# Performance work log

Hardware: AMD Instinct MI355X
Metric: run time of the kernel (lower is better)

## Reference

```python
import jax, jax.numpy as jnp
import numpy as np

DIM = 1024
NUM_HEADS = 16
HEAD_DIM = DIM // NUM_HEADS
SCALE = HEAD_DIM ** -0.5


def setup_inputs() -> dict:
    key = jax.random.key(0)
    k1, k2, k3, k4, k5, k6 = jax.random.split(key, 6)
    B, S, L = 4, 8192, 512
    x = jax.random.normal(k1, (B, S, DIM), dtype=jnp.float32)
    latents = jax.random.normal(k2, (B, L, DIM), dtype=jnp.float32)
    # Linear weights stored torch-style as (out_features, in_features)
    w_q = jax.random.normal(k3, (DIM, DIM), dtype=jnp.float32) * (DIM ** -0.5)
    w_kv = jax.random.normal(k4, (2 * DIM, DIM), dtype=jnp.float32) * (DIM ** -0.5)
    w_out = jax.random.normal(k5, (DIM, DIM), dtype=jnp.float32) * (DIM ** -0.5)
    b_out = jax.random.normal(k6, (DIM,), dtype=jnp.float32) * 0.01
    return {"x": x, "latents": latents, "w_q": w_q, "w_kv": w_kv,
            "w_out": w_out, "b_out": b_out}


def reference(x, latents, w_q, w_kv, w_out, b_out):
    B, L, _ = latents.shape
    S = x.shape[1]
    q = latents @ w_q.T                      # (B, L, dim)
    kv = x @ w_kv.T                          # (B, S, 2*dim)
    k, v = jnp.split(kv, 2, axis=-1)         # each (B, S, dim)
    q = q.reshape(B, L, NUM_HEADS, HEAD_DIM)
    k = k.reshape(B, S, NUM_HEADS, HEAD_DIM)
    v = v.reshape(B, S, NUM_HEADS, HEAD_DIM)
    # attention scores: (B, H, L, S)
    attn = jnp.einsum('blhd,bshd->bhls', q, k) * SCALE
    attn = jax.nn.softmax(attn, axis=-1)
    out = jnp.einsum('bhls,bshd->blhd', attn, v)  # (B, L, H, D)
    out = out.reshape(B, L, DIM)
    return out @ w_out.T + b_out
```

## Files before the change

kernel.cpp:

```cpp
#include <hip/hip_runtime.h>
#include <hip/hip_bf16.h>
#include <cstdint>
#include <cstddef>

#define B_ 4
#define S_ 8192
#define L_ 512
#define DIM 1024
#define NUM_HEADS 16
#define HEAD_DIM 64
#define SCHUNK 4096
#define NSEG 2
#define SEGKEYS (SCHUNK / NSEG)
#define SCALE 0.125f
#define L2E 1.44269504088896f
#define F_SC (SCALE * L2E)

typedef __bf16 bf16;
typedef __bf16 bf16x8 __attribute__((ext_vector_type(8)));
typedef float f32x4 __attribute__((ext_vector_type(4)));

#define AS1 __attribute__((address_space(1)))
#define AS3 __attribute__((address_space(3)))
#define GLDS(g, l) __builtin_amdgcn_global_load_lds((const AS1 void*)(g), (AS3 void*)(l), 16, 0, 0)
#define LGKM_FENCE() asm volatile("s_waitcnt lgkmcnt(0)" ::: "memory")
#define VMCNT4() asm volatile("s_waitcnt vmcnt(4)" ::: "memory")
#define VMCNT0() asm volatile("s_waitcnt vmcnt(0)" ::: "memory")
#define MFMA16(a, b, c) __builtin_amdgcn_mfma_f32_16x16x32_bf16((a), (b), (c), 0, 0, 0)

__global__ void detect_dtype(const unsigned int* __restrict__ x, int* __restrict__ flag) {
  int lane = threadIdx.x;
  int cnt = 0;
  for (int i = 0; i < 4; ++i) {
    unsigned int w = x[lane * 4 + i];
    unsigned int e = (w >> 7) & 0xFFu;
    cnt += (e >= 117u && e <= 129u) ? 1 : 0;
  }
  cnt += __shfl_xor(cnt, 1);
  cnt += __shfl_xor(cnt, 2);
  cnt += __shfl_xor(cnt, 4);
  cnt += __shfl_xor(cnt, 8);
  cnt += __shfl_xor(cnt, 16);
  cnt += __shfl_xor(cnt, 32);
  if (lane == 0) *flag = (cnt < 128) ? 1 : 0;
}

template<int REMAP>
__global__ __launch_bounds__(256) void conv_bf16(
    const void* __restrict__ in, bf16* __restrict__ out, int nchunk, int srow0,
    const int* __restrict__ flagp)
{
  const bool f32in = (*flagp != 0);
  for (int c = blockIdx.x * 256 + threadIdx.x; c < nchunk; c += gridDim.x * 256) {
    size_t gc;
    if (REMAP) {
      int r = c >> 7, cc = c & 127;
      gc = ((size_t)((r >> 12) * 8192 + srow0 + (r & 4095)) << 7) + cc;
    } else {
      gc = (size_t)c;
    }
    if (f32in) {
      const f32x4* g = (const f32x4*)in + gc * 2;
      f32x4 lo = g[0], hi = g[1];
      bf16x8 w;
      w[0] = (bf16)lo[0]; w[1] = (bf16)lo[1]; w[2] = (bf16)lo[2]; w[3] = (bf16)lo[3];
      w[4] = (bf16)hi[0]; w[5] = (bf16)hi[1]; w[6] = (bf16)hi[2]; w[7] = (bf16)hi[3];
      *(bf16x8*)(out + (size_t)c * 8) = w;
    } else {
      *(bf16x8*)(out + (size_t)c * 8) = ((const bf16x8*)in)[gc];
    }
  }
}

template<int HAS_BIAS, int DUAL_OUT, int NBN>
__global__ __launch_bounds__(256) void gemm_nt(
    const bf16* __restrict__ Ap, const bf16* __restrict__ Bwp,
    void* __restrict__ Cp, const void* __restrict__ biasp,
    int M, int N, int K, const int* __restrict__ flagp)
{
  __shared__ __align__(16) bf16 lA[128 * 64];
  __shared__ __align__(16) bf16 lB[128 * 64];
  const int tid = threadIdx.x;
  const int lane = tid & 63, quad = lane >> 4, l16 = lane & 15, wave = tid >> 6;
  const int wm = wave >> 1, wn = wave & 1;
  const int f = blockIdx.x;
  const int xcd = f & 7, sidx = f >> 3;
  const int bn = sidx % NBN;
  const int bm = xcd * (M >> 10) + sidx / NBN;
  const bool f32in = (HAS_BIAS || DUAL_OUT) ? (*flagp != 0) : false;

  f32x4 acc[4][4] = {};
  const int nK = K >> 6;
  for (int kb = 0; kb < nK; ++kb) {
    __syncthreads();
#pragma unroll
    for (int i = 0; i < 4; ++i) {
      int e = i * 256 + tid;
      int row = e >> 3, cp = e & 7, gcp = cp ^ (row & 7);
      const bf16* ga = Ap + (size_t)(bm * 128 + row) * K + kb * 64 + gcp * 8;
      GLDS(ga, lA + e * 8);
      const bf16* gb = Bwp + (size_t)(bn * 128 + row) * K + kb * 64 + gcp * 8;
      GLDS(gb, lB + e * 8);
    }
    __syncthreads();

#pragma unroll
    for (int ks = 0; ks < 2; ++ks) {
      bf16x8 af[4], bfr[4];
#pragma unroll
      for (int t = 0; t < 4; ++t) {
        int rowA = wm * 64 + t * 16 + l16;
        int ca = (ks * 4 + quad) ^ (rowA & 7);
        af[t] = *(const bf16x8*)(lA + rowA * 64 + ca * 8);
        int rowB = wn * 64 + t * 16 + l16;
        int cb = (ks * 4 + quad) ^ (rowB & 7);
        bfr[t] = *(const bf16x8*)(lB + rowB * 64 + cb * 8);
      }
#pragma unroll
      for (int tm = 0; tm < 4; ++tm)
#pragma unroll
        for (int tn = 0; tn < 4; ++tn)
          acc[tm][tn] = MFMA16(af[tm], bfr[tn], acc[tm][tn]);
    }
  }

#pragma unroll
  for (int tn = 0; tn < 4; ++tn) {
    int col = bn * 128 + wn * 64 + tn * 16 + l16;
    float bv = 0.0f;
    if (HAS_BIAS)
      bv = f32in ? ((const float*)biasp)[col] : (float)((const bf16*)biasp)[col];
#pragma unroll
    for (int tm = 0; tm < 4; ++tm) {
#pragma unroll
      for (int r = 0; r < 4; ++r) {
        int rowc = bm * 128 + wm * 64 + tm * 16 + quad * 4 + r;
        float v = acc[tm][tn][r] + bv;
        if (DUAL_OUT && f32in) {
          ((float*)Cp)[(size_t)rowc * N + col] = v;
        } else {
          ((bf16*)Cp)[(size_t)rowc * N + col] = (bf16)v;
        }
      }
    }
  }
}

__global__ __launch_bounds__(512) void gemm_kv_256(
    const bf16* __restrict__ Ap, const bf16* __restrict__ Bwp,
    bf16* __restrict__ Cp, bf16* __restrict__ C2p, int M, int K)
{
  __shared__ __align__(16) bf16 lA[2][256 * 64];
  __shared__ __align__(16) bf16 lB[2][256 * 64];
  const int tid = threadIdx.x;
  const int lane = tid & 63, quad = lane >> 4, l16 = lane & 15, wave = tid >> 6;
  const int wm = wave >> 2, wn = wave & 3;
  const int f = blockIdx.x;
  const int xcd = f & 7, sidx = f >> 3;
  const int bn = sidx & 7;
  const int bm = xcd * ((M >> 8) >> 3) + (sidx >> 3);
  const int nK = K >> 6;

#define STAGE_A(buf, half, kb) do {                                          \
  _Pragma("unroll")                                                          \
  for (int j = 0; j < 2; ++j) {                                              \
    int e = j * 512 + tid;                                                   \
    int row = e >> 3, cp = e & 7, gcp = cp ^ (row & 7);                      \
    const bf16* g = Ap + (size_t)(bm * 256 + (half) * 128 + row) * K         \
                       + (kb) * 64 + gcp * 8;                                \
    GLDS(g, &lA[buf][((half) * 128 + row) * 64 + cp * 8]);                   \
  } } while (0)
#define STAGE_B(buf, half, kb) do {                                          \
  _Pragma("unroll")                                                          \
  for (int j = 0; j < 2; ++j) {                                              \
    int e = j * 512 + tid;                                                   \
    int row = e >> 3, cp = e & 7, gcp = cp ^ (row & 7);                      \
    const bf16* g = Bwp + (size_t)(bn * 256 + (half) * 128 + row) * K        \
                        + (kb) * 64 + gcp * 8;                               \
    GLDS(g, &lB[buf][((half) * 128 + row) * 64 + cp * 8]);                   \
  } } while (0)

  f32x4 acc[8][4] = {};

  STAGE_A(0, 0, 0); STAGE_A(0, 1, 0); STAGE_B(0, 0, 0); STAGE_B(0, 1, 0);
  if (nK > 1) { STAGE_B(1, 0, 1); STAGE_B(1, 1, 1); VMCNT4(); }
  else VMCNT0();
  __builtin_amdgcn_s_barrier();

  for (int t = 0; t < nK; ++t) {
    const int cur = t & 1;
    bf16x8 breg[4][2];
#pragma unroll
    for (int p = 0; p < 4; ++p) {
      bf16x8 af[2][2];
      if (p == 0) {
#pragma unroll
        for (int nf = 0; nf < 4; ++nf)
#pragma unroll
          for (int ks = 0; ks < 2; ++ks) {
            int rowB = wn * 64 + nf * 16 + l16;
            int cb = (ks * 4 + quad) ^ (rowB & 7);
            breg[nf][ks] = *(const bf16x8*)&lB[cur][rowB * 64 + cb * 8];
          }
      }
#pragma unroll
      for (int mf2 = 0; mf2 < 2; ++mf2)
#pragma unroll
        for (int ks = 0; ks < 2; ++ks) {
          int rowA = wm * 128 + (p * 2 + mf2) * 16 + l16;
          int ca = (ks * 4 + quad) ^ (rowA & 7);
          af[mf2][ks] = *(const bf16x8*)&lA[cur][rowA * 64 + ca * 8];
        }
      LGKM_FENCE();

      if (p == 0) { if (t + 1 < nK) STAGE_A(cur ^ 1, 0, t + 1); }
      else if (p == 1) { if (t + 1 < nK) STAGE_A(cur ^ 1, 1, t + 1); }
      else if (p == 2) { if (t + 2 < nK) STAGE_B(cur, 0, t + 2); }
      else             { if (t + 2 < nK) STAGE_B(cur, 1, t + 2); }

      __builtin_amdgcn_s_barrier();

      __builtin_amdgcn_s_setprio(1);
#pragma unroll
      for (int mf2 = 0; mf2 < 2; ++mf2)
#pragma unroll
        for (int nf = 0; nf < 4; ++nf)
#pragma unroll
          for (int ks = 0; ks < 2; ++ks)
            acc[p * 2 + mf2][nf] = MFMA16(af[mf2][ks], breg[nf][ks], acc[p * 2 + mf2][nf]);
      __builtin_amdgcn_s_setprio(0);
    }
    if (t + 1 < nK) {
      if (t + 2 < nK) VMCNT4(); else VMCNT0();
      __builtin_amdgcn_s_barrier();
    }
  }

#pragma unroll
  for (int tn = 0; tn < 4; ++tn) {
    int col = bn * 256 + wn * 64 + tn * 16 + l16;
    bf16* outp = (col < 1024) ? Cp : C2p;
    int ocol = col & 1023;
#pragma unroll
    for (int tm = 0; tm < 8; ++tm)
#pragma unroll
      for (int r = 0; r < 4; ++r) {
        int rowc = bm * 256 + wm * 128 + tm * 16 + quad * 4 + r;
        outp[(size_t)rowc * 1024 + ocol] = (bf16)acc[tm][tn][r];
      }
  }
#undef STAGE_A
#undef STAGE_B
}

template<int FIRST>
__global__ __launch_bounds__(256) void attn_pass(
    const bf16* __restrict__ qb, const bf16* __restrict__ kc, const bf16* __restrict__ vc,
    float* __restrict__ Ost, float* __restrict__ lst)
{
  __shared__ __align__(16) bf16 lK[64 * 64];
  __shared__ __align__(16) bf16 lV[64][72];
  __shared__ __align__(16) bf16 pbuf[4][16][72];
  const int tid = threadIdx.x;
  const int lane = tid & 63, quad = lane >> 4, l16 = lane & 15, wave = tid >> 6;
  const int f = blockIdx.x;
  const int xcd = f & 7, sidx = f >> 3;
  const int lt = sidx & 7, ghi = sidx >> 3;
  const int g = ghi * 8 + xcd;
  const int h = g & 15, bs = g >> 4;
  const int b = bs >> 1, seg = bs & 1;
  const int l0 = lt * 64 + wave * 16;

  const bf16* qbase = qb + (size_t)(b * L_ + l0 + l16) * DIM + h * HEAD_DIM + quad * 8;
  bf16x8 qf0 = *(const bf16x8*)qbase;
  bf16x8 qf1 = *(const bf16x8*)(qbase + 32);

  f32x4 acc[4] = {};
  float lsum[4] = {0.0f, 0.0f, 0.0f, 0.0f};

  const int sbeg = seg * SEGKEYS;
  for (int s0 = sbeg; s0 < sbeg + SEGKEYS; s0 += 64) {
    __syncthreads();
    for (int i = 0; i < 2; ++i) {
      int e = i * 256 + tid;
      int row = e >> 3, cp = e & 7, gcp = cp ^ (row & 7);
      const bf16* gk = kc + (size_t)(b * SCHUNK + s0 + row) * DIM + h * HEAD_DIM + gcp * 8;
      GLDS(gk, lK + e * 8);
    }
    for (int i = 0; i < 2; ++i) {
      int e = i * 256 + tid;
      int row = e >> 3, cc = e & 7;
      bf16x8 vv = *(const bf16x8*)(vc + (size_t)(b * SCHUNK + s0 + row) * DIM + h * HEAD_DIM + cc * 8);
      int pg = (row >> 3) ^ cc;
#pragma unroll
      for (int j = 0; j < 8; ++j)
        lV[cc * 8 + j][pg * 8 + (row & 7)] = vv[j];
    }
    __syncthreads();

    f32x4 sc[4];
#pragma unroll
    for (int kt = 0; kt < 4; ++kt) {
      int rk = kt * 16 + l16;
      int p0c = quad ^ (rk & 7);
      int p1c = (4 + quad) ^ (rk & 7);
      bf16x8 kf0 = *(const bf16x8*)(lK + rk * 64 + p0c * 8);
      bf16x8 kf1 = *(const bf16x8*)(lK + rk * 64 + p1c * 8);
      f32x4 s4 = {};
      s4 = MFMA16(qf0, kf0, s4);
      s4 = MFMA16(qf1, kf1, s4);
      sc[kt] = s4;
    }

#pragma unroll
    for (int r = 0; r < 4; ++r) {
      float a0 = exp2f(fminf(sc[0][r] * F_SC, 40.0f));
      float a1 = exp2f(fminf(sc[1][r] * F_SC, 40.0f));
      float a2 = exp2f(fminf(sc[2][r] * F_SC, 40.0f));
      float a3 = exp2f(fminf(sc[3][r] * F_SC, 40.0f));
      lsum[r] += a0 + a1 + a2 + a3;
      pbuf[wave][quad * 4 + r][l16]      = (bf16)a0;
      pbuf[wave][quad * 4 + r][16 + l16] = (bf16)a1;
      pbuf[wave][quad * 4 + r][32 + l16] = (bf16)a2;
      pbuf[wave][quad * 4 + r][48 + l16] = (bf16)a3;
    }
    LGKM_FENCE();
#pragma unroll
    for (int half = 0; half < 2; ++half) {
      bf16x8 pf = *(const bf16x8*)&pbuf[wave][l16][half * 32 + quad * 8];
#pragma unroll
      for (int t4 = 0; t4 < 4; ++t4) {
        int c = t4 * 16 + l16;
        int pg = (half * 4 + quad) ^ (c >> 3);
        bf16x8 vf = *(const bf16x8*)&lV[c][pg * 8];
        acc[t4] = MFMA16(pf, vf, acc[t4]);
      }
    }
  }

#pragma unroll
  for (int r = 0; r < 4; ++r) {
    lsum[r] += __shfl_xor(lsum[r], 1, 16);
    lsum[r] += __shfl_xor(lsum[r], 2, 16);
    lsum[r] += __shfl_xor(lsum[r], 4, 16);
    lsum[r] += __shfl_xor(lsum[r], 8, 16);
  }

  float* Oseg = Ost + (size_t)seg * (B_ * L_ * DIM);
  float* lseg = lst + (size_t)seg * (B_ * NUM_HEADS * L_);
#pragma unroll
  for (int r = 0; r < 4; ++r) {
    int l = l0 + quad * 4 + r;
    if (l16 == 0) {
      int si = (b * NUM_HEADS + h) * L_ + l;
      if (FIRST) lseg[si] = lsum[r];
      else       lseg[si] += lsum[r];
    }
  }
#pragma unroll
  for (int t4 = 0; t4 < 4; ++t4)
#pragma unroll
    for (int r = 0; r < 4; ++r) {
      int l = l0 + quad * 4 + r;
      size_t oi = (size_t)(b * L_ + l) * DIM + h * HEAD_DIM + t4 * 16 + l16;
      if (FIRST) Oseg[oi] = acc[t4][r];
      else       Oseg[oi] += acc[t4][r];
    }
}

__global__ __launch_bounds__(256) void combine_kernel(
    const float* __restrict__ Ost, const float* __restrict__ lst, bf16* __restrict__ ao)
{
  int idx = (blockIdx.x * 256 + threadIdx.x) * 4;
  int d0 = idx & (DIM - 1);
  int row = idx >> 10;
  int b = row >> 9, l = row & (L_ - 1);
  int h = d0 >> 6;
  int si = (b * NUM_HEADS + h) * L_ + l;
  float lv = lst[si] + lst[B_ * NUM_HEADS * L_ + si];
  float linv = 1.0f / lv;
  f32x4 o0 = *(const f32x4*)(Ost + idx);
  f32x4 o1 = *(const f32x4*)(Ost + (size_t)(B_ * L_ * DIM) + idx);
#pragma unroll
  for (int j = 0; j < 4; ++j)
    ao[idx + j] = (bf16)((o0[j] + o1[j]) * linv);
}

extern "C" void kernel_launch(void* const* d_in, const int* in_sizes, int n_in,
                              void* d_out, int out_size, void* d_ws, size_t ws_size,
                              hipStream_t stream)
{
  (void)in_sizes; (void)n_in; (void)out_size; (void)ws_size;
  const void* x       = d_in[0];
  const void* latents = d_in[1];
  const void* w_q     = d_in[2];
  const void* w_kv    = d_in[3];
  const void* w_out   = d_in[4];
  const void* b_out   = d_in[5];

  char* ws = (char*)d_ws;
  int*   flag  = (int*)ws;
  bf16*  qb    = (bf16*)(ws + ((size_t)1   << 20));
  float* lst   = (float*)(ws + ((size_t)5  << 20));
  bf16*  ao    = (bf16*)(ws + ((size_t)6   << 20));
  float* Ost   = (float*)(ws + ((size_t)10 << 20));
  bf16*  kc    = (bf16*)(ws + ((size_t)26 << 20));
  bf16*  latb  = (bf16*)(ws + ((size_t)26 << 20));
  bf16*  wqb   = (bf16*)(ws + ((size_t)30 << 20));
  bf16*  vc    = (bf16*)(ws + ((size_t)58 << 20));
  bf16*  xcb   = (bf16*)(ws + ((size_t)90 << 20));
  bf16*  wkvb  = (bf16*)(ws + ((size_t)122 << 20));
  bf16*  woutb = (bf16*)(ws + ((size_t)122 << 20));

  detect_dtype<<<1, 64, 0, stream>>>((const unsigned int*)x, flag);

  const int Mx = B_ * SCHUNK;

  conv_bf16<0><<<1024, 256, 0, stream>>>(latents, latb, (B_ * L_ * DIM) / 8, 0, flag);
  conv_bf16<0><<<512,  256, 0, stream>>>(w_q, wqb, (DIM * DIM) / 8, 0, flag);
  conv_bf16<0><<<1024, 256, 0, stream>>>(w_kv, wkvb, (2 * DIM * DIM) / 8, 0, flag);

  gemm_nt<0, 0, 8><<<128, 256, 0, stream>>>(
      latb, wqb, qb, nullptr, B_ * L_, DIM, DIM, flag);

  conv_bf16<1><<<2048, 256, 0, stream>>>(x, xcb, (Mx * DIM) / 8, 0, flag);
  gemm_kv_256<<<512, 512, 0, stream>>>(xcb, wkvb, kc, vc, Mx, DIM);
  attn_pass<1><<<1024, 256, 0, stream>>>(qb, kc, vc, Ost, lst);

  conv_bf16<1><<<2048, 256, 0, stream>>>(x, xcb, (Mx * DIM) / 8, SCHUNK, flag);
  gemm_kv_256<<<512, 512, 0, stream>>>(xcb, wkvb, kc, vc, Mx, DIM);
  attn_pass<0><<<1024, 256, 0, stream>>>(qb, kc, vc, Ost, lst);

  conv_bf16<0><<<512, 256, 0, stream>>>(w_out, woutb, (DIM * DIM) / 8, 0, flag);
  combine_kernel<<<(B_ * L_ * DIM / 4) / 256, 256, 0, stream>>>(Ost, lst, ao);

  gemm_nt<1, 1, 8><<<128, 256, 0, stream>>>(
      ao, woutb, d_out, b_out, B_ * L_, DIM, DIM, flag);
}
```

Measured before the change: 567.9 us.

## Write V transposed from KV GEMM and double-buffer K/V loads in attention

The KV GEMM epilogue now writes V in a head-major transposed layout (b,h,d,s) with packed 4-element stores, so attention can load V tiles straight into LDS with async global-to-LDS loads instead of register loads followed by scattered transposing LDS writes. The attention loop double-buffers K and V tiles, prefetching the next tile while computing on the current one and using one barrier per iteration. This removes the per-element LDS transpose and overlaps global loads with MFMA work, at the cost of doubled LDS for K/V. The transposed V stores in the GEMM epilogue are strided across rows, which may make that store less coalesced.

```diff
diff --git a/kernel.cpp b/kernel.cpp
--- a/kernel.cpp
+++ b/kernel.cpp
@@ -18,6 +18,7 @@
 
 typedef __bf16 bf16;
 typedef __bf16 bf16x8 __attribute__((ext_vector_type(8)));
+typedef __bf16 bf16x4 __attribute__((ext_vector_type(4)));
 typedef float f32x4 __attribute__((ext_vector_type(4)));
 
 #define AS1 __attribute__((address_space(1)))
@@ -236,18 +237,33 @@
     }
   }
 
-#pragma unroll
-  for (int tn = 0; tn < 4; ++tn) {
-    int col = bn * 256 + wn * 64 + tn * 16 + l16;
-    bf16* outp = (col < 1024) ? Cp : C2p;
-    int ocol = col & 1023;
-#pragma unroll
-    for (int tm = 0; tm < 8; ++tm)
-#pragma unroll
-      for (int r = 0; r < 4; ++r) {
-        int rowc = bm * 256 + wm * 128 + tm * 16 + quad * 4 + r;
-        outp[(size_t)rowc * 1024 + ocol] = (bf16)acc[tm][tn][r];
+  if (bn < 4) {
+#pragma unroll
+    for (int tn = 0; tn < 4; ++tn) {
+      int col = bn * 256 + wn * 64 + tn * 16 + l16;
+#pragma unroll
+      for (int tm = 0; tm < 8; ++tm)
+#pragma unroll
+        for (int r = 0; r < 4; ++r) {
+          int rowc = bm * 256 + wm * 128 + tm * 16 + quad * 4 + r;
+          Cp[(size_t)rowc * 1024 + col] = (bf16)acc[tm][tn][r];
+        }
+    }
+  } else {
+#pragma unroll
+    for (int tn = 0; tn < 4; ++tn) {
+      int dv = bn * 256 + wn * 64 + tn * 16 + l16 - 1024;
+      int hh = dv >> 6, dd = dv & 63;
+#pragma unroll
+      for (int tm = 0; tm < 8; ++tm) {
+        int rowbase = bm * 256 + wm * 128 + tm * 16 + quad * 4;
+        int bb = rowbase >> 12, ss = rowbase & 4095;
+        bf16x4 pk;
+        pk[0] = (bf16)acc[tm][tn][0]; pk[1] = (bf16)acc[tm][tn][1];
+        pk[2] = (bf16)acc[tm][tn][2]; pk[3] = (bf16)acc[tm][tn][3];
+        *(bf16x4*)&C2p[(((size_t)((bb * 16 + hh) * 64 + dd)) << 12) + ss] = pk;
       }
+    }
   }
 #undef STAGE_A
 #undef STAGE_B
@@ -255,11 +271,11 @@
 
 template<int FIRST>
 __global__ __launch_bounds__(256) void attn_pass(
-    const bf16* __restrict__ qb, const bf16* __restrict__ kc, const bf16* __restrict__ vc,
+    const bf16* __restrict__ qb, const bf16* __restrict__ kc, const bf16* __restrict__ vt,
     float* __restrict__ Ost, float* __restrict__ lst)
 {
-  __shared__ __align__(16) bf16 lK[64 * 64];
-  __shared__ __align__(16) bf16 lV[64][72];
+  __shared__ __align__(16) bf16 lK[2][64 * 64];
+  __shared__ __align__(16) bf16 lV[2][64 * 64];
   __shared__ __align__(16) bf16 pbuf[4][16][72];
   const int tid = threadIdx.x;
   const int lane = tid & 63, quad = lane >> 4, l16 = lane & 15, wave = tid >> 6;
@@ -270,33 +286,37 @@
   const int h = g & 15, bs = g >> 4;
   const int b = bs >> 1, seg = bs & 1;
   const int l0 = lt * 64 + wave * 16;
+  const int sbeg = seg * SEGKEYS;
 
   const bf16* qbase = qb + (size_t)(b * L_ + l0 + l16) * DIM + h * HEAD_DIM + quad * 8;
   bf16x8 qf0 = *(const bf16x8*)qbase;
   bf16x8 qf1 = *(const bf16x8*)(qbase + 32);
 
+  const int r0 = tid >> 3, c0 = tid & 7, g0 = c0 ^ (r0 & 7);
+  const bf16* kg = kc + (((size_t)(b * SCHUNK + sbeg + r0)) << 10) + h * HEAD_DIM + g0 * 8;
+  const bf16* vg = vt + (((size_t)((b * 16 + h) * 64 + r0)) << 12) + sbeg + g0 * 8;
+
   f32x4 acc[4] = {};
   float lsum[4] = {0.0f, 0.0f, 0.0f, 0.0f};
 
-  const int sbeg = seg * SEGKEYS;
-  for (int s0 = sbeg; s0 < sbeg + SEGKEYS; s0 += 64) {
-    __syncthreads();
-    for (int i = 0; i < 2; ++i) {
-      int e = i * 256 + tid;
-      int row = e >> 3, cp = e & 7, gcp = cp ^ (row & 7);
-      const bf16* gk = kc + (size_t)(b * SCHUNK + s0 + row) * DIM + h * HEAD_DIM + gcp * 8;
-      GLDS(gk, lK + e * 8);
-    }
-    for (int i = 0; i < 2; ++i) {
-      int e = i * 256 + tid;
-      int row = e >> 3, cc = e & 7;
-      bf16x8 vv = *(const bf16x8*)(vc + (size_t)(b * SCHUNK + s0 + row) * DIM + h * HEAD_DIM + cc * 8);
-      int pg = (row >> 3) ^ cc;
-#pragma unroll
-      for (int j = 0; j < 8; ++j)
-        lV[cc * 8 + j][pg * 8 + (row & 7)] = vv[j];
-    }
-    __syncthreads();
+  {
+    bf16* lk = lK[0]; bf16* lv = lV[0];
+    GLDS(kg, lk + tid * 8); GLDS(kg + (32 << 10), lk + (256 + tid) * 8);
+    GLDS(vg, lv + tid * 8); GLDS(vg + (32 << 12), lv + (256 + tid) * 8);
+    kg += (64 << 10); vg += 64;
+  }
+  VMCNT0();
+  __syncthreads();
+
+  const int NT = SEGKEYS / 64;
+  for (int t = 0; t < NT; ++t) {
+    const int cur = t & 1;
+    if (t + 1 < NT) {
+      bf16* lk = lK[cur ^ 1]; bf16* lv = lV[cur ^ 1];
+      GLDS(kg, lk + tid * 8); GLDS(kg + (32 << 10), lk + (256 + tid) * 8);
+      GLDS(vg, lv + tid * 8); GLDS(vg + (32 << 12), lv + (256 + tid) * 8);
+      kg += (64 << 10); vg += 64;
+    }
 
     f32x4 sc[4];
 #pragma unroll
@@ -304,8 +324,8 @@
       int rk = kt * 16 + l16;
       int p0c = quad ^ (rk & 7);
       int p1c = (4 + quad) ^ (rk & 7);
-      bf16x8 kf0 = *(const bf16x8*)(lK + rk * 64 + p0c * 8);
-      bf16x8 kf1 = *(const bf16x8*)(lK + rk * 64 + p1c * 8);
+      bf16x8 kf0 = *(const bf16x8*)&lK[cur][rk * 64 + p0c * 8];
+      bf16x8 kf1 = *(const bf16x8*)&lK[cur][rk * 64 + p1c * 8];
       f32x4 s4 = {};
       s4 = MFMA16(qf0, kf0, s4);
       s4 = MFMA16(qf1, kf1, s4);
@@ -330,12 +350,15 @@
       bf16x8 pf = *(const bf16x8*)&pbuf[wave][l16][half * 32 + quad * 8];
 #pragma unroll
       for (int t4 = 0; t4 < 4; ++t4) {
-        int c = t4 * 16 + l16;
-        int pg = (half * 4 + quad) ^ (c >> 3);
-        bf16x8 vf = *(const bf16x8*)&lV[c][pg * 8];
+        int d = t4 * 16 + l16;
+        int cp = (half * 4 + quad) ^ (d & 7);
+        bf16x8 vf = *(const bf16x8*)&lV[cur][d * 64 + cp * 8];
         acc[t4] = MFMA16(pf, vf, acc[t4]);
       }
     }
+
+    VMCNT0();
+    __syncthreads();
   }
 
 #pragma unroll
@@ -407,7 +430,7 @@
   bf16*  kc    = (bf16*)(ws + ((size_t)26 << 20));
   bf16*  latb  = (bf16*)(ws + ((size_t)26 << 20));
   bf16*  wqb   = (bf16*)(ws + ((size_t)30 << 20));
-  bf16*  vc    = (bf16*)(ws + ((size_t)58 << 20));
+  bf16*  vt    = (bf16*)(ws + ((size_t)58 << 20));
   bf16*  xcb   = (bf16*)(ws + ((size_t)90 << 20));
   bf16*  wkvb  = (bf16*)(ws + ((size_t)122 << 20));
   bf16*  woutb = (bf16*)(ws + ((size_t)122 << 20));
@@ -424,12 +447,12 @@
       latb, wqb, qb, nullptr, B_ * L_, DIM, DIM, flag);
 
   conv_bf16<1><<<2048, 256, 0, stream>>>(x, xcb, (Mx * DIM) / 8, 0, flag);
-  gemm_kv_256<<<512, 512, 0, stream>>>(xcb, wkvb, kc, vc, Mx, DIM);
-  attn_pass<1><<<1024, 256, 0, stream>>>(qb, kc, vc, Ost, lst);
+  gemm_kv_256<<<512, 512, 0, stream>>>(xcb, wkvb, kc, vt, Mx, DIM);
+  attn_pass<1><<<1024, 256, 0, stream>>>(qb, kc, vt, Ost, lst);
 
   conv_bf16<1><<<2048, 256, 0, stream>>>(x, xcb, (Mx * DIM) / 8, SCHUNK, flag);
-  gemm_kv_256<<<512, 512, 0, stream>>>(xcb, wkvb, kc, vc, Mx, DIM);
-  attn_pass<0><<<1024, 256, 0, stream>>>(qb, kc, vc, Ost, lst);
+  gemm_kv_256<<<512, 512, 0, stream>>>(xcb, wkvb, kc, vt, Mx, DIM);
+  attn_pass<0><<<1024, 256, 0, stream>>>(qb, kc, vt, Ost, lst);
 
   conv_bf16<0><<<512, 256, 0, stream>>>(w_out, woutb, (DIM * DIM) / 8, 0, flag);
   combine_kernel<<<(B_ * L_ * DIM / 4) / 256, 256, 0, stream>>>(Ost, lst, ao);
```

Result: slower. 605.2 us (+6.6%).

## Split attention key tile across wave pairs with LDS reduction, double grid

Applied to the files above, without the earlier changes.

Each attention block now covers 32 query rows instead of 64, and the four waves form two query-tiles times two key-halves. Each wave processes half of every 64-key tile, and the partial outputs and row sums are reduced through shared memory before the write-out. The launch grid doubles to 2048 blocks, which adds parallelism and shortens per-wave work. The cost is that K/V tiles are loaded twice as often overall (once per 32 query rows instead of per 64), plus an extra LDS reduction and barrier at the end.

```diff
diff --git a/kernel.cpp b/kernel.cpp
--- a/kernel.cpp
+++ b/kernel.cpp
@@ -258,18 +258,20 @@
     const bf16* __restrict__ qb, const bf16* __restrict__ kc, const bf16* __restrict__ vc,
     float* __restrict__ Ost, float* __restrict__ lst)
 {
-  __shared__ __align__(16) bf16 lK[64 * 64];
-  __shared__ __align__(16) bf16 lV[64][72];
-  __shared__ __align__(16) bf16 pbuf[4][16][72];
+  __shared__ __align__(16) char smem[22528];
+  bf16* lK = (bf16*)smem;
+  bf16 (*lV)[72] = (bf16(*)[72])(smem + 8192);
   const int tid = threadIdx.x;
   const int lane = tid & 63, quad = lane >> 4, l16 = lane & 15, wave = tid >> 6;
+  const int qt = wave & 1, kh = wave >> 1;
+  bf16* pb = (bf16*)(smem + 17408) + wave * (16 * 40);
   const int f = blockIdx.x;
   const int xcd = f & 7, sidx = f >> 3;
-  const int lt = sidx & 7, ghi = sidx >> 3;
+  const int lt = sidx & 15, ghi = sidx >> 4;
   const int g = ghi * 8 + xcd;
   const int h = g & 15, bs = g >> 4;
   const int b = bs >> 1, seg = bs & 1;
-  const int l0 = lt * 64 + wave * 16;
+  const int l0 = lt * 32 + qt * 16;
 
   const bf16* qbase = qb + (size_t)(b * L_ + l0 + l16) * DIM + h * HEAD_DIM + quad * 8;
   bf16x8 qf0 = *(const bf16x8*)qbase;
@@ -298,10 +300,10 @@
     }
     __syncthreads();
 
-    f32x4 sc[4];
-#pragma unroll
-    for (int kt = 0; kt < 4; ++kt) {
-      int rk = kt * 16 + l16;
+    f32x4 sc[2];
+#pragma unroll
+    for (int kk = 0; kk < 2; ++kk) {
+      int rk = (kh * 2 + kk) * 16 + l16;
       int p0c = quad ^ (rk & 7);
       int p1c = (4 + quad) ^ (rk & 7);
       bf16x8 kf0 = *(const bf16x8*)(lK + rk * 64 + p0c * 8);
@@ -309,29 +311,24 @@
       f32x4 s4 = {};
       s4 = MFMA16(qf0, kf0, s4);
       s4 = MFMA16(qf1, kf1, s4);
-      sc[kt] = s4;
+      sc[kk] = s4;
     }
 
 #pragma unroll
     for (int r = 0; r < 4; ++r) {
       float a0 = exp2f(fminf(sc[0][r] * F_SC, 40.0f));
       float a1 = exp2f(fminf(sc[1][r] * F_SC, 40.0f));
-      float a2 = exp2f(fminf(sc[2][r] * F_SC, 40.0f));
-      float a3 = exp2f(fminf(sc[3][r] * F_SC, 40.0f));
-      lsum[r] += a0 + a1 + a2 + a3;
-      pbuf[wave][quad * 4 + r][l16]      = (bf16)a0;
-      pbuf[wave][quad * 4 + r][16 + l16] = (bf16)a1;
-      pbuf[wave][quad * 4 + r][32 + l16] = (bf16)a2;
-      pbuf[wave][quad * 4 + r][48 + l16] = (bf16)a3;
+      lsum[r] += a0 + a1;
+      pb[(quad * 4 + r) * 40 + l16]      = (bf16)a0;
+      pb[(quad * 4 + r) * 40 + 16 + l16] = (bf16)a1;
     }
     LGKM_FENCE();
-#pragma unroll
-    for (int half = 0; half < 2; ++half) {
-      bf16x8 pf = *(const bf16x8*)&pbuf[wave][l16][half * 32 + quad * 8];
+    {
+      bf16x8 pf = *(const bf16x8*)&pb[l16 * 40 + quad * 8];
 #pragma unroll
       for (int t4 = 0; t4 < 4; ++t4) {
         int c = t4 * 16 + l16;
-        int pg = (half * 4 + quad) ^ (c >> 3);
+        int pg = (kh * 4 + quad) ^ (c >> 3);
         bf16x8 vf = *(const bf16x8*)&lV[c][pg * 8];
         acc[t4] = MFMA16(pf, vf, acc[t4]);
       }
@@ -346,26 +343,51 @@
     lsum[r] += __shfl_xor(lsum[r], 8, 16);
   }
 
-  float* Oseg = Ost + (size_t)seg * (B_ * L_ * DIM);
-  float* lseg = lst + (size_t)seg * (B_ * NUM_HEADS * L_);
-#pragma unroll
-  for (int r = 0; r < 4; ++r) {
-    int l = l0 + quad * 4 + r;
-    if (l16 == 0) {
-      int si = (b * NUM_HEADS + h) * L_ + l;
-      if (FIRST) lseg[si] = lsum[r];
-      else       lseg[si] += lsum[r];
-    }
-  }
-#pragma unroll
-  for (int t4 = 0; t4 < 4; ++t4)
+  __syncthreads();
+  float* redA = (float*)smem;
+  float* redL = (float*)(smem + 8704);
+  if (kh == 1) {
+    float* pa = redA + (qt * 64 + lane) * 17;
+#pragma unroll
+    for (int t4 = 0; t4 < 4; ++t4)
+#pragma unroll
+      for (int r = 0; r < 4; ++r) pa[t4 * 4 + r] = acc[t4][r];
+    float* pl = redL + (qt * 64 + lane) * 4;
+#pragma unroll
+    for (int r = 0; r < 4; ++r) pl[r] = lsum[r];
+  }
+  __syncthreads();
+  if (kh == 0) {
+    float* pa = redA + (qt * 64 + lane) * 17;
+    float* pl = redL + (qt * 64 + lane) * 4;
+#pragma unroll
+    for (int t4 = 0; t4 < 4; ++t4)
+#pragma unroll
+      for (int r = 0; r < 4; ++r) acc[t4][r] += pa[t4 * 4 + r];
+#pragma unroll
+    for (int r = 0; r < 4; ++r) lsum[r] += pl[r];
+
+    float* Oseg = Ost + (size_t)seg * (B_ * L_ * DIM);
+    float* lseg = lst + (size_t)seg * (B_ * NUM_HEADS * L_);
 #pragma unroll
     for (int r = 0; r < 4; ++r) {
       int l = l0 + quad * 4 + r;
-      size_t oi = (size_t)(b * L_ + l) * DIM + h * HEAD_DIM + t4 * 16 + l16;
-      if (FIRST) Oseg[oi] = acc[t4][r];
-      else       Oseg[oi] += acc[t4][r];
-    }
+      if (l16 == 0) {
+        int si = (b * NUM_HEADS + h) * L_ + l;
+        if (FIRST) lseg[si] = lsum[r];
+        else       lseg[si] += lsum[r];
+      }
+    }
+#pragma unroll
+    for (int t4 = 0; t4 < 4; ++t4)
+#pragma unroll
+      for (int r = 0; r < 4; ++r) {
+        int l = l0 + quad * 4 + r;
+        size_t oi = (size_t)(b * L_ + l) * DIM + h * HEAD_DIM + t4 * 16 + l16;
+        if (FIRST) Oseg[oi] = acc[t4][r];
+        else       Oseg[oi] += acc[t4][r];
+      }
+  }
 }
 
 __global__ __launch_bounds__(256) void combine_kernel(
@@ -425,11 +447,11 @@
 
   conv_bf16<1><<<2048, 256, 0, stream>>>(x, xcb, (Mx * DIM) / 8, 0, flag);
   gemm_kv_256<<<512, 512, 0, stream>>>(xcb, wkvb, kc, vc, Mx, DIM);
-  attn_pass<1><<<1024, 256, 0, stream>>>(qb, kc, vc, Ost, lst);
+  attn_pass<1><<<2048, 256, 0, stream>>>(qb, kc, vc, Ost, lst);
 
   conv_bf16<1><<<2048, 256, 0, stream>>>(x, xcb, (Mx * DIM) / 8, SCHUNK, flag);
   gemm_kv_256<<<512, 512, 0, stream>>>(xcb, wkvb, kc, vc, Mx, DIM);
-  attn_pass<0><<<1024, 256, 0, stream>>>(qb, kc, vc, Ost, lst);
+  attn_pass<0><<<2048, 256, 0, stream>>>(qb, kc, vc, Ost, lst);
 
   conv_bf16<0><<<512, 256, 0, stream>>>(w_out, woutb, (DIM * DIM) / 8, 0, flag);
   combine_kernel<<<(B_ * L_ * DIM / 4) / 256, 256, 0, stream>>>(Ost, lst, ao);
```

Measured after the change: 621.7 us. 9.5% more time.
